# Kernel optimization log

Measured on AMD Instinct MI355X. Metric: run time of the kernel, lower is better.

The kernel has to match this reference:

```python
import jax, jax.numpy as jnp
import numpy as np

TEMPERATURE = 0.2

def setup_inputs() -> dict:
    key = jax.random.key(0)
    k1, k2 = jax.random.split(key)
    projected = jax.random.normal(k1, (2048, 2, 256), dtype=jnp.float32)
    predicted = jax.random.normal(k2, (2048, 4, 256), dtype=jnp.float32)
    return {"projected": projected, "predicted": predicted}

def _l2norm(x, eps=1e-12):
    n = jnp.linalg.norm(x, axis=-1, keepdims=True)
    return x / jnp.maximum(n, eps)

def reference(projected, predicted):
    # projected: [B, Vg, D], predicted: [B, Vt, D], Vt >= Vg.
    # Single-process: all_gather is identity, rank=0 -> labels = arange(B).
    B, Vg, D = projected.shape
    Vt = predicted.shape[1]
    Vl = Vt - Vg
    p = _l2norm(projected)
    q = _l2norm(predicted)
    # All pairwise similarity matrices at once: [Vg, Vt, B, B]
    logits = jnp.einsum('bid,cjd->ijbc', p, q) / TEMPERATURE
    lse = jax.nn.logsumexpr if False else jax.scipy.special.logsumexp(logits, axis=-1)  # [Vg, Vt, B]
    diag = jnp.diagonal(logits, axis1=-2, axis2=-1)                                    # [Vg, Vt, B]
    L = jnp.mean(lse - diag, axis=-1)  # per-pair CE loss, shape [Vg, Vt]
    # global terms: i != ii, both in [0, Vg)
    global_sum = jnp.sum(L[:, :Vg] * (1.0 - jnp.eye(Vg, dtype=L.dtype)))
    num_global_terms = Vg * (Vg - 1)
    global_loss = global_sum / num_global_terms if num_global_terms > 0 else jnp.float32(0.0)
    # local terms: faithful to source -> predicted columns 0..Vl-1 (not offset)
    num_local_terms = Vg * Vl
    local_sum = jnp.sum(L[:, :Vl]) if Vl > 0 else jnp.float32(0.0)
    local_loss = local_sum / num_local_terms if num_local_terms > 0 else jnp.float32(0.0)
    num_terms = num_global_terms + num_local_terms
    total = (global_sum + local_sum) / num_terms
    return (total, global_loss, local_loss)
```

## Files before the change

kernel.cpp:

```cpp
#include <hip/hip_runtime.h>
#include <hip/hip_bf16.h>
#include <hip/hip_fp8.h>
#include <stdint.h>

#define TB 2048
#define TD 256

typedef long long                                         fp8x8;
typedef __attribute__((ext_vector_type(16))) float        f32x16;

#define SQRT5 2.23606797749979f

__global__ __launch_bounds__(256) void nnclr_prep(const float* __restrict__ proj,
                                                  const float* __restrict__ pred,
                                                  unsigned char* __restrict__ pq2) {
    const int grp = blockIdx.x;
    const int v   = blockIdx.y;
    const int t   = threadIdx.x;

    __shared__ float rowbuf[32][261];
    __shared__ float scales[32];

    float x[32];
    #pragma unroll
    for (int m = 0; m < 32; ++m) {
        const int b = grp * 32 + m;
        const float* src = (v < 2) ? proj + ((size_t)b * 2 + v) * TD
                                   : pred + ((size_t)b * 4 + (v - 2)) * TD;
        x[m] = src[t];
    }
    #pragma unroll
    for (int m = 0; m < 32; ++m) rowbuf[m][t] = x[m];
    __syncthreads();

    {
        const int row = t >> 3, l8 = t & 7;
        float ss = 0.f;
        #pragma unroll
        for (int n = 0; n < 32; ++n) { const float y = rowbuf[row][l8 + 8 * n]; ss += y * y; }
        ss += __shfl_xor(ss, 1, 64);
        ss += __shfl_xor(ss, 2, 64);
        ss += __shfl_xor(ss, 4, 64);
        if (l8 == 0) scales[row] = SQRT5 / fmaxf(sqrtf(ss), 1e-12f);
    }
    __syncthreads();

    unsigned int* dst32 = (unsigned int*)(pq2 + (size_t)(v * 64 + grp) * 8192);
    #pragma unroll
    for (int it = 0; it < 8; ++it) {
        const int u   = it * 256 + t;
        const int m   = u >> 6;
        const int col = (u >> 1) & 31;
        const int e4  = u & 1;
        const float sc = scales[col];
        unsigned int w = 0;
        #pragma unroll
        for (int i = 0; i < 4; ++i) {
            const float y = rowbuf[col][m * 8 + 4 * e4 + i] * sc;
            const __hip_fp8_e4m3 f8(y);
            w |= ((unsigned int)f8.__x) << (8 * i);
        }
        dst32[u] = w;
    }
}

__global__ __launch_bounds__(256, 2) void nnclr_main(const unsigned char* __restrict__ pq2,
                                                     float* __restrict__ sPart,
                                                     float* __restrict__ dPart)
{
    const int rb = blockIdx.x, ch = blockIdx.y, j = blockIdx.z;
    const int tid = threadIdx.x, lane = tid & 63, wave = tid >> 6;
    const int cl = lane & 31, hk = lane >> 5;
    const int b0 = rb * 32;

    const fp8x8* P = (const fp8x8*)pq2;
    fp8x8 aF0[16], aF1[16];
    #pragma unroll
    for (int ks = 0; ks < 16; ++ks) {
        const int g = 2 * ks + hk;
        aF0[ks] = P[((0 * 64 + rb) * 32 + g) * 32 + cl];
        aF1[ks] = P[((1 * 64 + rb) * 32 + g) * 32 + cl];
    }

    float sAcc0[16], sAcc1[16];
    #pragma unroll
    for (int r = 0; r < 16; ++r) { sAcc0[r] = 0.f; sAcc1[r] = 0.f; }
    float d0 = 0.f, d1 = 0.f;
    const int  rDiag    = (cl & 3) + 4 * (cl >> 3);
    const bool laneDiag = (((cl >> 2) & 1) == hk);

    const fp8x8* Bbase = P + (size_t)(2 + j) * 64 * 32 * 32;
    const int cg0 = ch * 16 + wave * 4;

    fp8x8 bq[8];
    #pragma unroll
    for (int k = 0; k < 8; ++k) bq[k] = Bbase[(cg0 * 32 + 2 * k + hk) * 32 + cl];

    #pragma unroll
    for (int cgl = 0; cgl < 4; ++cgl) {
        const int cg = cg0 + cgl;
        f32x16 acc0, acc1;
        #pragma unroll
        for (int r = 0; r < 16; ++r) { acc0[r] = 0.f; acc1[r] = 0.f; }
        #pragma unroll
        for (int ks = 0; ks < 16; ++ks) {
            const fp8x8 b = bq[ks & 7];
            if (ks < 8)        bq[ks & 7] = Bbase[(cg * 32 + 2 * (ks + 8) + hk) * 32 + cl];
            else if (cgl < 3)  bq[ks & 7] = Bbase[((cg + 1) * 32 + 2 * (ks - 8) + hk) * 32 + cl];
            acc0 = __builtin_amdgcn_mfma_f32_32x32x16_fp8_fp8(aF0[ks], b, acc0, 0, 0, 0);
            acc1 = __builtin_amdgcn_mfma_f32_32x32x16_fp8_fp8(aF1[ks], b, acc1, 0, 0, 0);
        }
        const bool diagCG = (cg == rb);
        #pragma unroll
        for (int r = 0; r < 16; ++r) {
            const float v0 = acc0[r], v1 = acc1[r];
            sAcc0[r] += __expf(v0 - 5.0f);
            sAcc1[r] += __expf(v1 - 5.0f);
            if (diagCG) {
                const bool m = laneDiag && (r == rDiag);
                d0 += m ? v0 : 0.f;
                d1 += m ? v1 : 0.f;
            }
        }
    }

    #pragma unroll
    for (int r = 0; r < 16; ++r) {
        float s0 = sAcc0[r], s1 = sAcc1[r];
        #pragma unroll
        for (int msk = 1; msk < 32; msk <<= 1) {
            s0 += __shfl_xor(s0, msk, 64);
            s1 += __shfl_xor(s1, msk, 64);
        }
        sAcc0[r] = s0; sAcc1[r] = s1;
    }

    __shared__ float sArr[2][4][32];
    __shared__ float dArr[2][4][32];
    if (cl == 0) {
        #pragma unroll
        for (int r = 0; r < 16; ++r) {
            const int rowl = (r & 3) + 8 * (r >> 2) + 4 * hk;
            sArr[0][wave][rowl] = sAcc0[r];
            sArr[1][wave][rowl] = sAcc1[r];
        }
    }
    if (laneDiag) { dArr[0][wave][cl] = d0; dArr[1][wave][cl] = d1; }
    __syncthreads();
    if (tid < 64) {
        const int i = tid >> 5, row = tid & 31;
        float s = 0.f, d = 0.f;
        #pragma unroll
        for (int w = 0; w < 4; ++w) { s += sArr[i][w][row]; d += dArr[i][w][row]; }
        const int pair = i * 2 + j;
        const int b = b0 + row;
        sPart[((size_t)pair * TB + b) * 4 + ch] = s;
        dPart[((size_t)pair * TB + b) * 4 + ch] = d;
    }
}

__global__ __launch_bounds__(256) void nnclr_final1(const float* __restrict__ sPart,
                                                    const float* __restrict__ dPart,
                                                    float* __restrict__ Lpart) {
    const int tid = threadIdx.x;
    const int item = blockIdx.x * 256 + tid;
    const float4 sv = ((const float4*)sPart)[item];
    const float4 dv = ((const float4*)dPart)[item];
    const float s = (sv.x + sv.y) + (sv.z + sv.w);
    const float d = (dv.x + dv.y) + (dv.z + dv.w);
    float L = 5.0f + logf(s) - d;
    #pragma unroll
    for (int m = 1; m < 64; m <<= 1) L += __shfl_xor(L, m, 64);
    __shared__ float wsum[4];
    const int lane = tid & 63, wave = tid >> 6;
    if (lane == 0) wsum[wave] = L;
    __syncthreads();
    if (tid == 0) Lpart[blockIdx.x] = (wsum[0] + wsum[1]) + (wsum[2] + wsum[3]);
}

__global__ __launch_bounds__(64) void nnclr_final2(const float* __restrict__ Lpart,
                                                   float* __restrict__ out) {
    const int t = threadIdx.x;
    float v = (t < 32) ? Lpart[t] : 0.f;
    v += __shfl_xor(v, 1, 64);
    v += __shfl_xor(v, 2, 64);
    v += __shfl_xor(v, 4, 64);
    const float L0 = __shfl(v, 0, 64)  * (1.0f / TB);
    const float L1 = __shfl(v, 8, 64)  * (1.0f / TB);
    const float L2 = __shfl(v, 16, 64) * (1.0f / TB);
    const float L3 = __shfl(v, 24, 64) * (1.0f / TB);
    if (t == 0) {
        const float gs = L1 + L2;
        const float ls = L0 + L1 + L2 + L3;
        out[0] = (gs + ls) / 6.0f;
        out[1] = gs * 0.5f;
        out[2] = ls * 0.25f;
    }
}

extern "C" void kernel_launch(void* const* d_in, const int* in_sizes, int n_in,
                              void* d_out, int out_size, void* d_ws, size_t ws_size,
                              hipStream_t stream) {
    const float* projected = (const float*)d_in[0];
    const float* predicted = (const float*)d_in[1];

    unsigned char* pq2 = (unsigned char*)d_ws;
    float* sPart = (float*)((char*)d_ws + 4u * 1024u * 1024u);
    float* dPart = sPart + (size_t)4 * TB * 4;
    float* Lpart = dPart + (size_t)4 * TB * 4;
    float* out = (float*)d_out;

    dim3 gprep(64, 4);
    nnclr_prep<<<gprep, 256, 0, stream>>>(projected, predicted, pq2);
    dim3 gmain(64, 4, 2);
    nnclr_main<<<gmain, 256, 0, stream>>>(pq2, sPart, dPart);
    nnclr_final1<<<32, 256, 0, stream>>>(sPart, dPart, Lpart);
    nnclr_final2<<<1, 64, 0, stream>>>(Lpart, out);
}
```

Measured before the change: 27.69 us.

## Merge final reduction kernels into one and vectorize prep loads

The two final reduction kernels are merged into a single 1024-thread block that reads all partial sums, keeps a per-pair accumulator for each of the four pairs, and writes the three outputs directly. This drops one kernel launch and the round trip through the Lpart buffer. The prep kernel now loads rows as float4 and stores them into shared memory as float4, with the row pitch changed to 260 to keep 16-byte alignment. The cost is that the final stage runs on one workgroup instead of 32, and the new row pitch may add shared-memory bank conflicts in the norm and fp8 packing reads.

```diff
diff --git a/kernel.cpp b/kernel.cpp
--- a/kernel.cpp
+++ b/kernel.cpp
@@ -18,19 +18,19 @@
     const int v   = blockIdx.y;
     const int t   = threadIdx.x;
 
-    __shared__ float rowbuf[32][261];
+    __shared__ float rowbuf[32][260];
     __shared__ float scales[32];
 
-    float x[32];
-    #pragma unroll
-    for (int m = 0; m < 32; ++m) {
+    #pragma unroll
+    for (int it = 0; it < 8; ++it) {
+        const int f = it * 256 + t;
+        const int m = f >> 6, q = f & 63;
         const int b = grp * 32 + m;
-        const float* src = (v < 2) ? proj + ((size_t)b * 2 + v) * TD
-                                   : pred + ((size_t)b * 4 + (v - 2)) * TD;
-        x[m] = src[t];
-    }
-    #pragma unroll
-    for (int m = 0; m < 32; ++m) rowbuf[m][t] = x[m];
+        const float4* src = (v < 2) ? (const float4*)(proj + ((size_t)b * 2 + v) * TD)
+                                    : (const float4*)(pred + ((size_t)b * 4 + (v - 2)) * TD);
+        const float4 val = src[q];
+        *(float4*)&rowbuf[m][q * 4] = val;
+    }
     __syncthreads();
 
     {
@@ -159,39 +159,42 @@
     }
 }
 
-__global__ __launch_bounds__(256) void nnclr_final1(const float* __restrict__ sPart,
+__global__ __launch_bounds__(1024) void nnclr_final(const float* __restrict__ sPart,
                                                     const float* __restrict__ dPart,
-                                                    float* __restrict__ Lpart) {
+                                                    float* __restrict__ out) {
     const int tid = threadIdx.x;
-    const int item = blockIdx.x * 256 + tid;
-    const float4 sv = ((const float4*)sPart)[item];
-    const float4 dv = ((const float4*)dPart)[item];
-    const float s = (sv.x + sv.y) + (sv.z + sv.w);
-    const float d = (dv.x + dv.y) + (dv.z + dv.w);
-    float L = 5.0f + logf(s) - d;
-    #pragma unroll
-    for (int m = 1; m < 64; m <<= 1) L += __shfl_xor(L, m, 64);
-    __shared__ float wsum[4];
+    float acc[4] = {0.f, 0.f, 0.f, 0.f};
+    #pragma unroll
+    for (int k = 0; k < 8; ++k) {
+        const int item = k * 1024 + tid;
+        const float4 sv = ((const float4*)sPart)[item];
+        const float4 dv = ((const float4*)dPart)[item];
+        const float s = (sv.x + sv.y) + (sv.z + sv.w);
+        const float d = (dv.x + dv.y) + (dv.z + dv.w);
+        acc[k >> 1] += 5.0f + logf(s) - d;
+    }
+    __shared__ float red[16][4];
     const int lane = tid & 63, wave = tid >> 6;
-    if (lane == 0) wsum[wave] = L;
-    __syncthreads();
-    if (tid == 0) Lpart[blockIdx.x] = (wsum[0] + wsum[1]) + (wsum[2] + wsum[3]);
-}
-
-__global__ __launch_bounds__(64) void nnclr_final2(const float* __restrict__ Lpart,
-                                                   float* __restrict__ out) {
-    const int t = threadIdx.x;
-    float v = (t < 32) ? Lpart[t] : 0.f;
-    v += __shfl_xor(v, 1, 64);
-    v += __shfl_xor(v, 2, 64);
-    v += __shfl_xor(v, 4, 64);
-    const float L0 = __shfl(v, 0, 64)  * (1.0f / TB);
-    const float L1 = __shfl(v, 8, 64)  * (1.0f / TB);
-    const float L2 = __shfl(v, 16, 64) * (1.0f / TB);
-    const float L3 = __shfl(v, 24, 64) * (1.0f / TB);
-    if (t == 0) {
-        const float gs = L1 + L2;
-        const float ls = L0 + L1 + L2 + L3;
+    #pragma unroll
+    for (int p = 0; p < 4; ++p) {
+        #pragma unroll
+        for (int m = 1; m < 64; m <<= 1) acc[p] += __shfl_xor(acc[p], m, 64);
+    }
+    if (lane == 0) {
+        #pragma unroll
+        for (int p = 0; p < 4; ++p) red[wave][p] = acc[p];
+    }
+    __syncthreads();
+    if (tid == 0) {
+        float L[4];
+        #pragma unroll
+        for (int p = 0; p < 4; ++p) {
+            float a = 0.f;
+            for (int w = 0; w < 16; ++w) a += red[w][p];
+            L[p] = a / (float)TB;
+        }
+        const float gs = L[1] + L[2];
+        const float ls = L[0] + L[1] + L[2] + L[3];
         out[0] = (gs + ls) / 6.0f;
         out[1] = gs * 0.5f;
         out[2] = ls * 0.25f;
@@ -207,13 +210,11 @@
     unsigned char* pq2 = (unsigned char*)d_ws;
     float* sPart = (float*)((char*)d_ws + 4u * 1024u * 1024u);
     float* dPart = sPart + (size_t)4 * TB * 4;
-    float* Lpart = dPart + (size_t)4 * TB * 4;
     float* out = (float*)d_out;
 
     dim3 gprep(64, 4);
     nnclr_prep<<<gprep, 256, 0, stream>>>(projected, predicted, pq2);
     dim3 gmain(64, 4, 2);
     nnclr_main<<<gmain, 256, 0, stream>>>(pq2, sPart, dPart);
-    nnclr_final1<<<32, 256, 0, stream>>>(sPart, dPart, Lpart);
-    nnclr_final2<<<1, 64, 0, stream>>>(Lpart, out);
-}
+    nnclr_final<<<1, 1024, 0, stream>>>(sPart, dPart, out);
+}
```

Result: no change. 28.03 us (+1.2%).
